# Performance work log

Hardware: AMD Instinct MI355X
Metric: run time of the kernel (lower is better)

## Reference

```python
import jax, jax.numpy as jnp
import numpy as np

SEQ, BATCH, D_MODEL = 2048, 2, 1024
NHEAD = 16
HEAD_DIM = D_MODEL // NHEAD
D_FF = 4096
LN_EPS = 1e-5
ROPE_THETA = 10000.0


def _rope_cos_sin(seq_len, dim, dtype):
    # lucidrains RotaryEmbedding: inv_freq over even indices, interleaved repeat
    inv_freq = 1.0 / (ROPE_THETA ** (jnp.arange(0, dim, 2, dtype=jnp.float32) / dim))
    t = jnp.arange(seq_len, dtype=jnp.float32)
    freqs = t[:, None] * inv_freq[None, :]            # [S, dim/2]
    freqs = jnp.repeat(freqs, 2, axis=-1)             # [S, dim] (f0,f0,f1,f1,...)
    return jnp.cos(freqs).astype(dtype), jnp.sin(freqs).astype(dtype)


def _rotate_half(x):
    # interleaved pairs: (x0,x1,x2,x3,...) -> (-x1,x0,-x3,x2,...)
    x = x.reshape(x.shape[:-1] + (-1, 2))
    x1, x2 = x[..., 0], x[..., 1]
    return jnp.stack([-x2, x1], axis=-1).reshape(x.shape[:-2] + (-1,))


def _apply_rope(x, cos, sin):
    # x: [B, H, S, D]; cos/sin: [S, D]
    return x * cos[None, None, :, :] + _rotate_half(x) * sin[None, None, :, :]


def _layer_norm(x, g, b):
    mu = jnp.mean(x, axis=-1, keepdims=True)
    var = jnp.mean(jnp.square(x - mu), axis=-1, keepdims=True)
    return (x - mu) * jax.lax.rsqrt(var + LN_EPS) * g + b


def setup_inputs() -> dict:
    key = jax.random.key(0)
    ks = jax.random.split(key, 12)
    s = 1.0 / np.sqrt(D_MODEL)
    sf = 1.0 / np.sqrt(D_FF)
    return {
        "src": jax.random.normal(ks[0], (SEQ, BATCH, D_MODEL), jnp.float32),
        "q_w": jax.random.uniform(ks[1], (D_MODEL, D_MODEL), jnp.float32, -s, s),
        "q_b": jnp.zeros((D_MODEL,), jnp.float32),
        "k_w": jax.random.uniform(ks[2], (D_MODEL, D_MODEL), jnp.float32, -s, s),
        "k_b": jnp.zeros((D_MODEL,), jnp.float32),
        "v_w": jax.random.uniform(ks[3], (D_MODEL, D_MODEL), jnp.float32, -s, s),
        "v_b": jnp.zeros((D_MODEL,), jnp.float32),
        "w1": jax.random.uniform(ks[4], (D_MODEL, D_FF), jnp.float32, -s, s),
        "b1": jnp.zeros((D_FF,), jnp.float32),
        "w2": jax.random.uniform(ks[5], (D_FF, D_MODEL), jnp.float32, -sf, sf),
        "b2": jnp.zeros((D_MODEL,), jnp.float32),
        "ln1_g": jnp.ones((D_MODEL,), jnp.float32),
        "ln1_b": jnp.zeros((D_MODEL,), jnp.float32),
        "ln2_g": jnp.ones((D_MODEL,), jnp.float32),
        "ln2_b": jnp.zeros((D_MODEL,), jnp.float32),
    }


def reference(src, q_w, q_b, k_w, k_b, v_w, v_b, w1, b1, w2, b2,
              ln1_g, ln1_b, ln2_g, ln2_b):
    S, B, E = src.shape
    q = src @ q_w + q_b
    k = src @ k_w + k_b
    v = src @ v_w + v_b
    # [S,B,E] -> [B,H,S,D]
    def split_heads(x):
        return x.reshape(S, B, NHEAD, HEAD_DIM).transpose(1, 2, 0, 3)
    q, k, v = split_heads(q), split_heads(k), split_heads(v)
    cos, sin = _rope_cos_sin(S, HEAD_DIM, src.dtype)
    q = _apply_rope(q, cos, sin)
    k = _apply_rope(k, cos, sin)
    scores = jnp.einsum("bhqd,bhkd->bhqk", q, k) / np.sqrt(HEAD_DIM)
    probs = jax.nn.softmax(scores, axis=-1)
    out = jnp.einsum("bhqk,bhkd->bhqd", probs, v)      # [B,H,S,D]
    out = out.transpose(2, 0, 1, 3).reshape(S, B, E)
    x = _layer_norm(src + out, ln1_g, ln1_b)
    ff = (jax.nn.relu(x @ w1 + b1)) @ w2 + b2
    return _layer_norm(x + ff, ln2_g, ln2_b)
```

## Files before the change

kernel.cpp:

```cpp
#include <hip/hip_runtime.h>
#include <hip/hip_bf16.h>

#define SEQ 2048
#define BATCH 2
#define DMODEL 1024
#define NHEAD 16
#define HDIM 64
#define DFF 4096
#define LN_EPS 1e-5f
#define QKVSZ (BATCH * NHEAD * SEQ * HDIM)

typedef unsigned short ushort_t;
typedef __attribute__((ext_vector_type(8))) short short8;
typedef __attribute__((ext_vector_type(4))) float floatx4;
typedef __attribute__((ext_vector_type(16))) float floatx16;

__device__ __forceinline__ float bf2f(ushort_t u) {
    union { unsigned int i; float f; } v;
    v.i = ((unsigned int)u) << 16;
    return v.f;
}
__device__ __forceinline__ ushort_t f2bf(float f) {
    union { float f; unsigned int i; } v;
    v.f = f;
    unsigned int r = v.i + 0x7fffu + ((v.i >> 16) & 1u);
    return (ushort_t)(r >> 16);
}
__device__ __forceinline__ unsigned int cvtpk_bf16(float lo, float hi) {
    unsigned int r;
    asm("v_cvt_pk_bf16_f32 %0, %1, %2" : "=v"(r) : "v"(lo), "v"(hi));
    return r;
}
__device__ __forceinline__ float fast_exp2(float x) {
    float r;
    asm("v_exp_f32 %0, %1" : "=v"(r) : "v"(x));
    return r;
}
__device__ __forceinline__ void gload_lds16(const ushort_t* g, ushort_t* l) {
    __builtin_amdgcn_global_load_lds(
        (const __attribute__((address_space(1))) void*)g,
        (__attribute__((address_space(3))) void*)l, 16, 0, 0);
}

__global__ __launch_bounds__(256) void sniff_kernel(const ushort_t* __restrict__ qw,
                                                    int* __restrict__ flag) {
    float mx = 0.f;
    for (int i = threadIdx.x; i < 4096; i += 256) {
        float v = fabsf(bf2f(qw[i]));
        if (v <= 3.0e38f) mx = fmaxf(mx, v);
    }
#pragma unroll
    for (int off = 1; off < 64; off <<= 1) mx = fmaxf(mx, __shfl_xor(mx, off, 64));
    __shared__ float sm[4];
    if ((threadIdx.x & 63) == 0) sm[threadIdx.x >> 6] = mx;
    __syncthreads();
    if (threadIdx.x == 0) {
        float m = fmaxf(fmaxf(sm[0], sm[1]), fmaxf(sm[2], sm[3]));
        *flag = (m > 1.0f) ? 1 : 0;
    }
}

__global__ __launch_bounds__(256) void convert_kernel(const void* __restrict__ src,
                                                      ushort_t* __restrict__ dst,
                                                      int n, const int* __restrict__ flag) {
    const int f = *flag;
    int i = blockIdx.x * 256 + threadIdx.x;
    const int stride = gridDim.x * 256;
    if (f) {
        const float* s = (const float*)src;
        for (; i < n; i += stride) dst[i] = f2bf(s[i]);
    } else {
        const ushort_t* s = (const ushort_t*)src;
        for (; i < n; i += stride) dst[i] = s[i];
    }
}

__global__ __launch_bounds__(256) void transpose_all_kernel(
    const void* __restrict__ s0, const void* __restrict__ s1,
    const void* __restrict__ s2, const void* __restrict__ s3,
    const void* __restrict__ s4,
    ushort_t* __restrict__ wqkvT, ushort_t* __restrict__ w1T,
    ushort_t* __restrict__ w2T, const int* __restrict__ flag)
{
    __shared__ ushort_t tile[64][72];
    const int id = blockIdx.x;
    const void* src; ushort_t* dst; int K, N, bx, by;
    if (id < 768) {
        int mat = id >> 8, t = id & 255;
        src = (mat == 0) ? s0 : ((mat == 1) ? s1 : s2);
        dst = wqkvT + (size_t)mat * DMODEL * DMODEL;
        K = DMODEL; N = DMODEL; bx = t & 15; by = t >> 4;
    } else if (id < 1792) {
        int t = id - 768;
        src = s3; dst = w1T; K = DMODEL; N = DFF; bx = t & 63; by = t >> 6;
    } else {
        int t = id - 1792;
        src = s4; dst = w2T; K = DFF; N = DMODEL; bx = t & 15; by = t >> 4;
    }
    const int n0 = bx * 64, k0 = by * 64;
    const int tx = threadIdx.x & 63, ty = threadIdx.x >> 6;
    const int f = *flag;
    if (f) {
        const float* s = (const float*)src;
#pragma unroll
        for (int i = 0; i < 16; i++) {
            int r = ty + 4 * i;
            tile[r][tx] = f2bf(s[(size_t)(k0 + r) * N + n0 + tx]);
        }
    } else {
        const ushort_t* s = (const ushort_t*)src;
#pragma unroll
        for (int i = 0; i < 16; i++) {
            int r = ty + 4 * i;
            tile[r][tx] = s[(size_t)(k0 + r) * N + n0 + tx];
        }
    }
    __syncthreads();
#pragma unroll
    for (int i = 0; i < 16; i++) {
        int r = ty + 4 * i;
        dst[(size_t)(n0 + r) * K + k0 + tx] = tile[tx][r];
    }
}

__global__ __launch_bounds__(256) void small_setup_kernel(
    const void* __restrict__ qb, const void* __restrict__ kb,
    const void* __restrict__ vb, const void* __restrict__ b1,
    const void* __restrict__ b2, const void* __restrict__ g1,
    const void* __restrict__ be1, const void* __restrict__ g2,
    const void* __restrict__ be2,
    char* __restrict__ sp, float* __restrict__ rope,
    const int* __restrict__ flag)
{
    const int i = blockIdx.x * 256 + threadIdx.x;
    if (i >= 12288) {
        int idx = i - 12288;
        int s = idx >> 5, ii = idx & 31;
        float inv = exp2f(-(float)(2 * ii) * (13.287712379549449f / 64.f));
        float ang = (float)s * inv;
        rope[idx * 2 + 0] = cosf(ang);
        rope[idx * 2 + 1] = sinf(ang);
        return;
    }
    const int f = *flag;
    const void* src; ushort_t* dst; int j;
    if (i < 3072)       { src = (i < 1024) ? qb : ((i < 2048) ? kb : vb);
                          j = i & 1023; dst = (ushort_t*)sp + i; }
    else if (i < 7168)  { src = b1;  j = i - 3072;  dst = (ushort_t*)(sp + 8192) + j; }
    else if (i < 8192)  { src = b2;  j = i - 7168;  dst = (ushort_t*)(sp + 16384) + j; }
    else if (i < 9216)  { src = g1;  j = i - 8192;  dst = (ushort_t*)(sp + 20480) + j; }
    else if (i < 10240) { src = be1; j = i - 9216;  dst = (ushort_t*)(sp + 24576) + j; }
    else if (i < 11264) { src = g2;  j = i - 10240; dst = (ushort_t*)(sp + 28672) + j; }
    else                { src = be2; j = i - 11264; dst = (ushort_t*)(sp + 32768) + j; }
    *dst = f ? f2bf(((const float*)src)[j]) : ((const ushort_t*)src)[j];
}

template <int MODE>
__global__ __launch_bounds__(256) void gemm_kernel(
    const ushort_t* __restrict__ A, const ushort_t* __restrict__ BT,
    const ushort_t* __restrict__ bias, void* __restrict__ out,
    void* __restrict__ out2, const float* __restrict__ rope,
    int M, int N, int K)
{
    __shared__ ushort_t sA[128 * 32];
    __shared__ ushort_t sB[128 * 32];

    const int tid = threadIdx.x;
    const int lane = tid & 63;
    const int w = tid >> 6;
    const int wm = (w >> 1) * 64;
    const int wn = (w & 1) * 64;
    const int m0 = blockIdx.y * 128;
    const int n0 = blockIdx.x * 128;

    const int Kc = (MODE == 3) ? (K >> 1) : K;
    const int kbeg = (MODE == 3) ? (int)blockIdx.z * Kc : 0;

    floatx4 acc[4][4];
#pragma unroll
    for (int i = 0; i < 4; i++)
#pragma unroll
        for (int j = 0; j < 4; j++) {
            floatx4 z = {0.f, 0.f, 0.f, 0.f};
            acc[i][j] = z;
        }

    const int srow = tid >> 2;
    const int scol = (tid & 3) * 8;
    const ushort_t* Ag = A + (size_t)(m0 + srow) * K + scol + kbeg;
    const ushort_t* Bg = BT + (size_t)(n0 + srow) * K + scol + kbeg;
    ushort_t* ldsA0 = sA + w * 512;
    ushort_t* ldsA1 = sA + 2048 + w * 512;
    ushort_t* ldsB0 = sB + w * 512;
    ushort_t* ldsB1 = sB + 2048 + w * 512;
    const size_t rstep = (size_t)64 * K;

    for (int k0 = 0; k0 < Kc; k0 += 32) {
        gload_lds16(Ag + k0, ldsA0);
        gload_lds16(Ag + rstep + k0, ldsA1);
        gload_lds16(Bg + k0, ldsB0);
        gload_lds16(Bg + rstep + k0, ldsB1);
        __syncthreads();

        short8 a[4], b[4];
#pragma unroll
        for (int mt = 0; mt < 4; mt++)
            a[mt] = *(const short8*)&sA[(wm + mt * 16 + (lane & 15)) * 32 + (lane >> 4) * 8];
#pragma unroll
        for (int nt = 0; nt < 4; nt++)
            b[nt] = *(const short8*)&sB[(wn + nt * 16 + (lane & 15)) * 32 + (lane >> 4) * 8];
#pragma unroll
        for (int mt = 0; mt < 4; mt++)
#pragma unroll
            for (int nt = 0; nt < 4; nt++)
                acc[mt][nt] = __builtin_amdgcn_mfma_f32_16x16x32_bf16(
                    a[mt], b[nt], acc[mt][nt], 0, 0, 0);
        __syncthreads();
    }

#pragma unroll
    for (int mt = 0; mt < 4; mt++) {
#pragma unroll
        for (int nt = 0; nt < 4; nt++) {
#pragma unroll
            for (int r = 0; r < 4; r++) {
                int row = wm + mt * 16 + (lane >> 4) * 4 + r;
                int col = wn + nt * 16 + (lane & 15);
                int m = m0 + row, n = n0 + col;
                float val = acc[mt][nt][r];
                if (MODE != 3) val += bf2f(bias[n]);
                if (MODE == 1) {
                    int mat = n >> 10, nn = n & 1023;
                    int h = nn >> 6, d = nn & 63;
                    int s = m >> 1, bb = m & 1;
                    if (mat < 2) {
                        int i = d >> 1;
                        float c  = rope[((size_t)s * 32 + i) * 2 + 0];
                        float sn = rope[((size_t)s * 32 + i) * 2 + 1];
                        float partner = __shfl_xor(val, 1, 64);
                        val = (d & 1) ? (val * c + partner * sn)
                                      : (val * c - partner * sn);
                        if (mat == 0) val *= 0.18033688011112042f;
                    }
                    size_t off;
                    if (mat == 2)
                        off = (size_t)2 * QKVSZ + ((size_t)(bb * NHEAD + h) * HDIM + d) * SEQ + s;
                    else
                        off = (size_t)mat * QKVSZ + ((size_t)(bb * NHEAD + h) * SEQ + s) * HDIM + d;
                    ((ushort_t*)out)[off] = f2bf(val);
                } else if (MODE == 2) {
                    ((ushort_t*)out)[(size_t)m * N + n] = f2bf(fmaxf(val, 0.f));
                } else {
                    float* outp = blockIdx.z ? (float*)out2 : (float*)out;
                    outp[(size_t)m * N + n] = val;
                }
            }
        }
    }
}

__global__ __launch_bounds__(256) void attn_kernel(
    const ushort_t* __restrict__ Q, const ushort_t* __restrict__ K,
    const ushort_t* __restrict__ VT, ushort_t* __restrict__ out)
{
    __shared__ ushort_t sQO[128][72];
    __shared__ ushort_t sK[2][64][72];
    __shared__ ushort_t sVT[2][64][72];

    const int tid  = threadIdx.x;
    const int lane = tid & 63;
    const int w    = tid >> 6;
    const int h    = lane >> 5;
    const int q5   = lane & 31;
    const int bh   = blockIdx.y;
    const int q0   = blockIdx.x * 128;

    const ushort_t* Qg  = Q + ((size_t)bh * SEQ + q0) * HDIM;
    const ushort_t* Kg  = K + (size_t)bh * SEQ * HDIM;
    const ushort_t* VTg = VT + (size_t)bh * SEQ * HDIM;

    const int sr0 = tid >> 3,          sc0 = (tid & 7) * 8;
    const int sr1 = (tid + 256) >> 3,  sc1 = ((tid + 256) & 7) * 8;

#pragma unroll
    for (int p = 0; p < 4; p++) {
        int chunk = tid + p * 256;
        int r = chunk >> 3, c = (chunk & 7) * 8;
        *(short8*)&sQO[r][c] = *(const short8*)(Qg + (size_t)r * HDIM + c);
    }
    *(short8*)&sK[0][sr0][sc0]  = *(const short8*)(Kg + (size_t)sr0 * HDIM + sc0);
    *(short8*)&sK[0][sr1][sc1]  = *(const short8*)(Kg + (size_t)sr1 * HDIM + sc1);
    *(short8*)&sVT[0][sr0][sc0] = *(const short8*)(VTg + (size_t)sr0 * SEQ + sc0);
    *(short8*)&sVT[0][sr1][sc1] = *(const short8*)(VTg + (size_t)sr1 * SEQ + sc1);
    __syncthreads();

    short8 qf[4];
#pragma unroll
    for (int kk = 0; kk < 4; kk++)
        qf[kk] = *(const short8*)&sQO[w * 32 + q5][kk * 16 + h * 8];

    floatx16 accO[2];
#pragma unroll
    for (int dt = 0; dt < 2; dt++)
#pragma unroll
        for (int r = 0; r < 16; r++) accO[dt][r] = 0.f;
    float accL = 0.f;

    for (int kv0 = 0; kv0 < SEQ; kv0 += 64) {
        const int cur = (kv0 >> 6) & 1;
        const bool has_next = (kv0 + 64) < SEQ;

        short8 gK0, gK1, gV0, gV1;
        if (has_next) {
            const ushort_t* Kn = Kg + (size_t)(kv0 + 64) * HDIM;
            gK0 = *(const short8*)(Kn + (size_t)sr0 * HDIM + sc0);
            gK1 = *(const short8*)(Kn + (size_t)sr1 * HDIM + sc1);
            gV0 = *(const short8*)(VTg + (size_t)sr0 * SEQ + kv0 + 64 + sc0);
            gV1 = *(const short8*)(VTg + (size_t)sr1 * SEQ + kv0 + 64 + sc1);
        }

        floatx16 accS[2];
#pragma unroll
        for (int t = 0; t < 2; t++) {
#pragma unroll
            for (int r = 0; r < 16; r++) accS[t][r] = 0.f;
#pragma unroll
            for (int kk = 0; kk < 4; kk++) {
                short8 aK = *(const short8*)&sK[cur][t * 32 + q5][kk * 16 + h * 8];
                accS[t] = __builtin_amdgcn_mfma_f32_32x32x16_bf16(
                    aK, qf[kk], accS[t], 0, 0, 0);
            }
        }

        unsigned int pa[2][4], pb[2][4];
        float l0 = 0.f, l1 = 0.f, l2 = 0.f, l3 = 0.f;
#pragma unroll
        for (int t = 0; t < 2; t++) {
#pragma unroll
            for (int r = 0; r < 16; r += 4) {
                accS[t][r + 0] = fast_exp2(accS[t][r + 0]);
                accS[t][r + 1] = fast_exp2(accS[t][r + 1]);
                accS[t][r + 2] = fast_exp2(accS[t][r + 2]);
                accS[t][r + 3] = fast_exp2(accS[t][r + 3]);
                l0 += accS[t][r + 0];
                l1 += accS[t][r + 1];
                l2 += accS[t][r + 2];
                l3 += accS[t][r + 3];
            }
#pragma unroll
            for (int s = 0; s < 4; s++) {
                pa[t][s] = cvtpk_bf16(accS[t][4 * s + 0], accS[t][4 * s + 1]);
                pb[t][s] = cvtpk_bf16(accS[t][4 * s + 2], accS[t][4 * s + 3]);
            }
        }
        accL += (l0 + l1) + (l2 + l3);

#pragma unroll
        for (int w4 = 0; w4 < 4; w4++) {
            const int t = w4 >> 1, wh = w4 & 1;
            unsigned int xa = pa[t][2 * wh + 1], ya = pa[t][2 * wh];
            unsigned int xb = pb[t][2 * wh + 1], yb = pb[t][2 * wh];
            asm volatile("v_permlane32_swap_b32 %0, %1" : "+v"(xa), "+v"(ya));
            asm volatile("v_permlane32_swap_b32 %0, %1" : "+v"(xb), "+v"(yb));
            union { unsigned int u[4]; short8 s; } bf;
            bf.u[0] = ya; bf.u[1] = yb; bf.u[2] = xa; bf.u[3] = xb;
#pragma unroll
            for (int dt = 0; dt < 2; dt++) {
                short8 aV = *(const short8*)&sVT[cur][dt * 32 + q5][w4 * 16 + h * 8];
                accO[dt] = __builtin_amdgcn_mfma_f32_32x32x16_bf16(
                    aV, bf.s, accO[dt], 0, 0, 0);
            }
        }

        if (has_next) {
            *(short8*)&sK[cur ^ 1][sr0][sc0]  = gK0;
            *(short8*)&sK[cur ^ 1][sr1][sc1]  = gK1;
            *(short8*)&sVT[cur ^ 1][sr0][sc0] = gV0;
            *(short8*)&sVT[cur ^ 1][sr1][sc1] = gV1;
        }
        __syncthreads();
    }

    accL += __shfl_xor(accL, 32, 64);
    float rinv = 1.0f / accL;

#pragma unroll
    for (int dt = 0; dt < 2; dt++)
#pragma unroll
        for (int r = 0; r < 16; r++) {
            int d = dt * 32 + (r & 3) + 8 * (r >> 2) + 4 * h;
            sQO[w * 32 + q5][d] = f2bf(accO[dt][r] * rinv);
        }

    const int b = bh >> 4, hd = bh & 15;
#pragma unroll
    for (int p = 0; p < 4; p++) {
        int rl = p * 8 + (lane >> 3);
        int c = (lane & 7) * 8;
        int qrow = q0 + w * 32 + rl;
        short8 v = *(const short8*)&sQO[w * 32 + rl][c];
        *(short8*)(out + ((size_t)qrow * BATCH + b) * DMODEL + hd * HDIM + c) = v;
    }
}

__global__ __launch_bounds__(256) void ln1_kernel(
    const ushort_t* __restrict__ src, ushort_t* io,
    const ushort_t* __restrict__ g, const ushort_t* __restrict__ bb)
{
    const int row = blockIdx.x;
    const int tid = threadIdx.x;
    const size_t base = (size_t)row * DMODEL;
    const int j0 = tid * 4;
    float v[4];
#pragma unroll
    for (int j = 0; j < 4; j++)
        v[j] = bf2f(src[base + j0 + j]) + bf2f(io[base + j0 + j]);

    float s = v[0] + v[1] + v[2] + v[3];
    float ss = v[0] * v[0] + v[1] * v[1] + v[2] * v[2] + v[3] * v[3];
#pragma unroll
    for (int off = 1; off < 64; off <<= 1) {
        s += __shfl_xor(s, off, 64);
        ss += __shfl_xor(ss, off, 64);
    }
    __shared__ float ps[4], pss[4];
    if ((tid & 63) == 0) { ps[tid >> 6] = s; pss[tid >> 6] = ss; }
    __syncthreads();
    s = ps[0] + ps[1] + ps[2] + ps[3];
    ss = pss[0] + pss[1] + pss[2] + pss[3];
    float mu = s * (1.f / DMODEL);
    float var = ss * (1.f / DMODEL) - mu * mu;
    float rstd = rsqrtf(var + LN_EPS);
#pragma unroll
    for (int j = 0; j < 4; j++) {
        float y = (v[j] - mu) * rstd * bf2f(g[j0 + j]) + bf2f(bb[j0 + j]);
        io[base + j0 + j] = f2bf(y);
    }
}

__global__ __launch_bounds__(256) void ln2_kernel(
    const ushort_t* __restrict__ xb, float* io,
    const float* __restrict__ ff1, const ushort_t* __restrict__ b2,
    const ushort_t* __restrict__ g, const ushort_t* __restrict__ bb)
{
    const int row = blockIdx.x;
    const int tid = threadIdx.x;
    const size_t base = (size_t)row * DMODEL;
    const int j0 = tid * 4;
    float v[4];
#pragma unroll
    for (int j = 0; j < 4; j++)
        v[j] = bf2f(xb[base + j0 + j]) + io[base + j0 + j] + ff1[base + j0 + j]
             + bf2f(b2[j0 + j]);

    float s = v[0] + v[1] + v[2] + v[3];
    float ss = v[0] * v[0] + v[1] * v[1] + v[2] * v[2] + v[3] * v[3];
#pragma unroll
    for (int off = 1; off < 64; off <<= 1) {
        s += __shfl_xor(s, off, 64);
        ss += __shfl_xor(ss, off, 64);
    }
    __shared__ float ps[4], pss[4];
    if ((tid & 63) == 0) { ps[tid >> 6] = s; pss[tid >> 6] = ss; }
    __syncthreads();
    s = ps[0] + ps[1] + ps[2] + ps[3];
    ss = pss[0] + pss[1] + pss[2] + pss[3];
    float mu = s * (1.f / DMODEL);
    float var = ss * (1.f / DMODEL) - mu * mu;
    float rstd = rsqrtf(var + LN_EPS);
#pragma unroll
    for (int j = 0; j < 4; j++) {
        float y = (v[j] - mu) * rstd * bf2f(g[j0 + j]) + bf2f(bb[j0 + j]);
        io[base + j0 + j] = y;
    }
}

extern "C" void kernel_launch(void* const* d_in, const int* in_sizes, int n_in,
                              void* d_out, int out_size, void* d_ws, size_t ws_size,
                              hipStream_t stream)
{
    char* ws = (char*)d_ws;
    const size_t MB = 1024 * 1024;
    const size_t KB = 1024;

    ushort_t* c_src   = (ushort_t*)(ws + 0);
    ushort_t* c_wqkvT = (ushort_t*)(ws + 8 * MB);
    ushort_t* c_w1T   = (ushort_t*)(ws + 14 * MB);
    ushort_t* c_w2T   = (ushort_t*)(ws + 22 * MB);
    char* sp = ws + 30 * MB;
    ushort_t* c_qkvb  = (ushort_t*)(sp + 0 * KB);
    ushort_t* c_b1    = (ushort_t*)(sp + 8 * KB);
    ushort_t* c_b2    = (ushort_t*)(sp + 16 * KB);
    ushort_t* c_ln1g  = (ushort_t*)(sp + 20 * KB);
    ushort_t* c_ln1b  = (ushort_t*)(sp + 24 * KB);
    ushort_t* c_ln2g  = (ushort_t*)(sp + 28 * KB);
    ushort_t* c_ln2b  = (ushort_t*)(sp + 32 * KB);
    int*      flag    = (int*)(sp + 36 * KB);
    float*    rope    = (float*)(ws + 30 * MB + 512 * KB);
    ushort_t* QKVb    = (ushort_t*)(ws + 31 * MB);
    ushort_t* attn_xb = (ushort_t*)(ws + 63 * MB);
    ushort_t* hbuf    = (ushort_t*)(ws + 31 * MB);
    float*    ffb1    = (float*)(ws + 0);
    float*    ffb0    = (float*)d_out;

    const int M = SEQ * BATCH;
    dim3 blk(256);

    sniff_kernel<<<dim3(1), blk, 0, stream>>>((const ushort_t*)d_in[1], flag);

    transpose_all_kernel<<<dim3(2816), blk, 0, stream>>>(
        d_in[1], d_in[3], d_in[5], d_in[7], d_in[9],
        c_wqkvT, c_w1T, c_w2T, flag);

    convert_kernel<<<dim3(2048), blk, 0, stream>>>(
        d_in[0], c_src, SEQ * BATCH * DMODEL, flag);

    small_setup_kernel<<<dim3(304), blk, 0, stream>>>(
        d_in[2], d_in[4], d_in[6], d_in[8], d_in[10],
        d_in[11], d_in[12], d_in[13], d_in[14],
        sp, rope, flag);

    gemm_kernel<1><<<dim3(3 * DMODEL / 128, M / 128), blk, 0, stream>>>(
        c_src, c_wqkvT, c_qkvb, QKVb, nullptr, rope, M, 3 * DMODEL, DMODEL);

    attn_kernel<<<dim3(SEQ / 128, BATCH * NHEAD), blk, 0, stream>>>(
        QKVb, QKVb + QKVSZ, QKVb + 2 * QKVSZ, attn_xb);

    ln1_kernel<<<dim3(M), blk, 0, stream>>>(c_src, attn_xb, c_ln1g, c_ln1b);

    gemm_kernel<2><<<dim3(DFF / 128, M / 128), blk, 0, stream>>>(
        attn_xb, c_w1T, c_b1, hbuf, nullptr, rope, M, DFF, DMODEL);

    gemm_kernel<3><<<dim3(DMODEL / 128, M / 128, 2), blk, 0, stream>>>(
        hbuf, c_w2T, c_b2, ffb0, ffb1, rope, M, DMODEL, DFF);

    ln2_kernel<<<dim3(M), blk, 0, stream>>>(attn_xb, ffb0, ffb1, c_b2, c_ln2g, c_ln2b);
}
```

Baseline: 368.4 us.

## Double GEMM K-step to 64 and swizzle workgroups across XCDs

The GEMM main loop now loads two 32-wide K slices per iteration into a doubled LDS buffer, which halves the number of barrier pairs per tile. Workgroup IDs are also remapped so that consecutive tiles land on the same XCD, aiming for better L2 reuse of shared A/B panels. The cost is twice the LDS per block, which may reduce occupancy. The swizzle ignores blockIdx.z, which is harmless for split-K because z only selects the K half.

```diff
diff --git a/kernel.cpp b/kernel.cpp
--- a/kernel.cpp
+++ b/kernel.cpp
@@ -162,16 +162,23 @@
     void* __restrict__ out2, const float* __restrict__ rope,
     int M, int N, int K)
 {
-    __shared__ ushort_t sA[128 * 32];
-    __shared__ ushort_t sB[128 * 32];
+    __shared__ ushort_t sA[2 * 128 * 32];
+    __shared__ ushort_t sB[2 * 128 * 32];
 
     const int tid = threadIdx.x;
     const int lane = tid & 63;
     const int w = tid >> 6;
     const int wm = (w >> 1) * 64;
     const int wn = (w & 1) * 64;
-    const int m0 = blockIdx.y * 128;
-    const int n0 = blockIdx.x * 128;
+
+    const int gx = gridDim.x;
+    const int nwg = gx * gridDim.y;
+    const int orig = blockIdx.y * gx + blockIdx.x;
+    const int qq = nwg >> 3, rr = nwg & 7;
+    const int xcd = orig & 7, idx8 = orig >> 3;
+    const int swz = (xcd < rr ? xcd * (qq + 1) : rr * (qq + 1) + (xcd - rr) * qq) + idx8;
+    const int m0 = (swz / gx) * 128;
+    const int n0 = (swz % gx) * 128;
 
     const int Kc = (MODE == 3) ? (K >> 1) : K;
     const int kbeg = (MODE == 3) ? (int)blockIdx.z * Kc : 0;
@@ -189,32 +196,34 @@
     const int scol = (tid & 3) * 8;
     const ushort_t* Ag = A + (size_t)(m0 + srow) * K + scol + kbeg;
     const ushort_t* Bg = BT + (size_t)(n0 + srow) * K + scol + kbeg;
-    ushort_t* ldsA0 = sA + w * 512;
-    ushort_t* ldsA1 = sA + 2048 + w * 512;
-    ushort_t* ldsB0 = sB + w * 512;
-    ushort_t* ldsB1 = sB + 2048 + w * 512;
     const size_t rstep = (size_t)64 * K;
 
-    for (int k0 = 0; k0 < Kc; k0 += 32) {
-        gload_lds16(Ag + k0, ldsA0);
-        gload_lds16(Ag + rstep + k0, ldsA1);
-        gload_lds16(Bg + k0, ldsB0);
-        gload_lds16(Bg + rstep + k0, ldsB1);
+    for (int k0 = 0; k0 < Kc; k0 += 64) {
+#pragma unroll
+        for (int c = 0; c < 2; c++) {
+            gload_lds16(Ag + k0 + 32 * c,         sA + c * 4096 + w * 512);
+            gload_lds16(Ag + rstep + k0 + 32 * c, sA + c * 4096 + 2048 + w * 512);
+            gload_lds16(Bg + k0 + 32 * c,         sB + c * 4096 + w * 512);
+            gload_lds16(Bg + rstep + k0 + 32 * c, sB + c * 4096 + 2048 + w * 512);
+        }
         __syncthreads();
 
-        short8 a[4], b[4];
-#pragma unroll
-        for (int mt = 0; mt < 4; mt++)
-            a[mt] = *(const short8*)&sA[(wm + mt * 16 + (lane & 15)) * 32 + (lane >> 4) * 8];
-#pragma unroll
-        for (int nt = 0; nt < 4; nt++)
-            b[nt] = *(const short8*)&sB[(wn + nt * 16 + (lane & 15)) * 32 + (lane >> 4) * 8];
-#pragma unroll
-        for (int mt = 0; mt < 4; mt++)
+#pragma unroll
+        for (int kk = 0; kk < 2; kk++) {
+            short8 a[4], b[4];
+#pragma unroll
+            for (int mt = 0; mt < 4; mt++)
+                a[mt] = *(const short8*)&sA[kk * 4096 + (wm + mt * 16 + (lane & 15)) * 32 + (lane >> 4) * 8];
 #pragma unroll
             for (int nt = 0; nt < 4; nt++)
-                acc[mt][nt] = __builtin_amdgcn_mfma_f32_16x16x32_bf16(
-                    a[mt], b[nt], acc[mt][nt], 0, 0, 0);
+                b[nt] = *(const short8*)&sB[kk * 4096 + (wn + nt * 16 + (lane & 15)) * 32 + (lane >> 4) * 8];
+#pragma unroll
+            for (int mt = 0; mt < 4; mt++)
+#pragma unroll
+                for (int nt = 0; nt < 4; nt++)
+                    acc[mt][nt] = __builtin_amdgcn_mfma_f32_16x16x32_bf16(
+                        a[mt], b[nt], acc[mt][nt], 0, 0, 0);
+        }
         __syncthreads();
     }
 
```

Result: faster. 351.0 us (-4.7%).
